# Optimization experiments

Measured on AMD Instinct MI355X. Metric: run time of the kernel, lower is better.

## Reference

```python
import jax, jax.numpy as jnp
import numpy as np

N, B, E = 2048, 2, 1024      # seq_len, batch, embedding_dims
H = 1024                      # hidden_dims
NH, D = 16, 64                # num_heads, head_dim (NH*D == H)
SCALE = 1.0 / float(np.sqrt(H))  # NOTE: module divides by sqrt(hidden_dims), not sqrt(head_dim)


def setup_inputs() -> dict:
    key = jax.random.key(0)
    k0, k1, k2 = jax.random.split(key, 3)
    x = jax.random.normal(k0, (N, B, E), dtype=jnp.float32)
    W_proj = jax.random.normal(k1, (E, 3 * H), dtype=jnp.float32) * 0.02
    b_proj = jnp.zeros((3 * H,), dtype=jnp.float32)
    W_out = jax.random.normal(k2, (H, E), dtype=jnp.float32) * 0.02
    b_out = jnp.zeros((E,), dtype=jnp.float32)
    return {"x": x, "W_proj": W_proj, "b_proj": b_proj, "W_out": W_out, "b_out": b_out}


def reference(x, W_proj, b_proj, W_out, b_out):
    n, b, _ = x.shape
    # QKV projection: [n, b, 3H] -> 'n b (k h d) -> k b h n d'
    proj = x @ W_proj + b_proj
    qkv = proj.reshape(n, b, 3, NH, D).transpose(2, 1, 3, 0, 4)  # [3, b, h, n, d]
    q, k, v = qkv[0], qkv[1], qkv[2]
    # scaled dot-product scores [b, h, n, n]
    scores = jnp.einsum('bhid,bhjd->bhij', q, k) * SCALE
    # causal mask: -inf above the diagonal (generate_square_subsequent_mask)
    i = jnp.arange(n)
    mask = jnp.where(i[None, :] > i[:, None], -jnp.inf, 0.0).astype(scores.dtype)
    att = jax.nn.softmax(scores + mask, axis=-1)  # dropout = identity (eval)
    out = jnp.einsum('bhij,bhjd->bhid', att, v)   # [b, h, n, d]
    out = out.transpose(2, 0, 1, 3).reshape(n, b, H)  # 'b h n d -> n b (h d)'
    return out @ W_out + b_out
```

## Files before the change

### kernel.cpp

```cpp
#include <hip/hip_runtime.h>
#include <cstdint>
#include <cstddef>

typedef __bf16 bf16_t;
typedef __bf16 bf16x8 __attribute__((ext_vector_type(8)));
typedef __bf16 bf16x4 __attribute__((ext_vector_type(4)));
typedef float f32x4 __attribute__((ext_vector_type(4)));

#define N_SEQ 2048
#define BATCH 2
#define EMB   1024
#define HID   1024
#define NHEAD 16
#define HDIM  64
#define NBROW (N_SEQ * BATCH)
#define ATT_SCALE2 (0.03125f * 1.44269504f)

#define EXP2F(x) __builtin_amdgcn_exp2f(x)

static __device__ __forceinline__ void async_copy16(const bf16_t* g, bf16_t* l) {
  __builtin_amdgcn_global_load_lds((const __attribute__((address_space(1))) void*)g,
                                   (__attribute__((address_space(3))) void*)l,
                                   16, 0, 0);
}

__global__ __launch_bounds__(256) void prep_kernel(
    const float* __restrict__ x, const float* __restrict__ Wp,
    const float* __restrict__ Wo, bf16_t* __restrict__ Xb,
    bf16_t* __restrict__ Wpt, bf16_t* __restrict__ Wot) {
  int bid = blockIdx.x;
  if (bid < 4096) {
    int i = (bid * 256 + threadIdx.x) * 4;
    float4 v = *(const float4*)(x + i);
    bf16x4 o;
    o[0] = (bf16_t)v.x; o[1] = (bf16_t)v.y; o[2] = (bf16_t)v.z; o[3] = (bf16_t)v.w;
    *(bf16x4*)(Xb + i) = o;
    return;
  }
  __shared__ float tile[32][33];
  const float* in; bf16_t* out; int R, C, bx;
  if (bid < 4096 + 3072) { bx = bid - 4096; in = Wp; out = Wpt; R = 1024; C = 3072; }
  else                   { bx = bid - 7168; in = Wo; out = Wot; R = 1024; C = 1024; }
  int gx = C / 32;
  int bc = (bx % gx) * 32, br = (bx / gx) * 32;
  int tx = threadIdx.x & 31, ty = threadIdx.x >> 5;
  #pragma unroll
  for (int i = 0; i < 32; i += 8)
    tile[ty + i][tx] = in[(size_t)(br + ty + i) * C + bc + tx];
  __syncthreads();
  #pragma unroll
  for (int i = 0; i < 32; i += 8)
    out[(size_t)(bc + ty + i) * R + br + tx] = (bf16_t)tile[tx][ty + i];
}

__global__ void vt_transpose_kernel(const bf16_t* __restrict__ Pj,
                                    bf16_t* __restrict__ Vt) {
  __shared__ bf16_t tile[32][33];
  int tx = threadIdx.x & 31, ty = threadIdx.x >> 5;
  int n0 = blockIdx.x * 32, d0 = blockIdx.y * 32;
  int bh = blockIdx.z;
  int h = bh & 15, b = bh >> 4;
  const int PJP = 3 * HID;
  #pragma unroll
  for (int i = 0; i < 32; i += 8)
    tile[ty + i][tx] = Pj[(size_t)((n0 + ty + i) * BATCH + b) * PJP + 2 * HID + h * HDIM + d0 + tx];
  __syncthreads();
  #pragma unroll
  for (int i = 0; i < 32; i += 8)
    Vt[(size_t)(bh * HDIM + d0 + ty + i) * N_SEQ + n0 + tx] = tile[tx][ty + i];
}

template <int BM, int BN, int BK, bool OUT_BF16, bool SCALEQ>
__global__ __launch_bounds__(256) void gemm_bt_kernel(
    const bf16_t* __restrict__ A, const bf16_t* __restrict__ Bt,
    const float* __restrict__ bias, void* __restrict__ Cout,
    int M, int Nn, int K) {
  constexpr int MT = BM / 32;
  constexpr int NT = BN / 32;
  constexpr int OCTS = BK / 8;
  constexpr int OM = OCTS - 1;
  __shared__ __align__(16) bf16_t As[BM * BK];
  __shared__ __align__(16) bf16_t Bs[BN * BK];
  int tid = threadIdx.x;
  int wave = tid >> 6, lane = tid & 63;
  int c = lane & 15, quad = lane >> 4;
  int bm = blockIdx.x * BM;
  int bn = blockIdx.y * BN;
  int wm = (wave & 1) * (BM / 2), wn = (wave >> 1) * (BN / 2);
  f32x4 acc[MT][NT] = {};

  for (int kb = 0; kb < K; kb += BK) {
    #pragma unroll
    for (int i = 0; i < BM * OCTS / 256; ++i) {
      int p = i * 256 + tid;
      int row = p >> (OCTS == 8 ? 3 : 4), ko = (p & OM) ^ (row & OM);
      async_copy16(A + (size_t)(bm + row) * K + kb + ko * 8,
                   As + (size_t)(i * 256 + wave * 64) * 8);
    }
    #pragma unroll
    for (int i = 0; i < BN * OCTS / 256; ++i) {
      int p = i * 256 + tid;
      int row = p >> (OCTS == 8 ? 3 : 4), ko = (p & OM) ^ (row & OM);
      async_copy16(Bt + (size_t)(bn + row) * K + kb + ko * 8,
                   Bs + (size_t)(i * 256 + wave * 64) * 8);
    }
    __syncthreads();
    #pragma unroll
    for (int kk = 0; kk < BK / 32; ++kk) {
      bf16x8 af[MT], bf[NT];
      #pragma unroll
      for (int mt = 0; mt < MT; ++mt) {
        int row = wm + mt * 16 + c;
        int slot = (kk * 4 + quad) ^ (row & OM);
        af[mt] = *(const bf16x8*)(As + (size_t)(row * OCTS + slot) * 8);
      }
      #pragma unroll
      for (int nt = 0; nt < NT; ++nt) {
        int row = wn + nt * 16 + c;
        int slot = (kk * 4 + quad) ^ (row & OM);
        bf[nt] = *(const bf16x8*)(Bs + (size_t)(row * OCTS + slot) * 8);
      }
      #pragma unroll
      for (int mt = 0; mt < MT; ++mt)
        #pragma unroll
        for (int nt = 0; nt < NT; ++nt)
          acc[mt][nt] = __builtin_amdgcn_mfma_f32_16x16x32_bf16(
              af[mt], bf[nt], acc[mt][nt], 0, 0, 0);
    }
    __syncthreads();
  }

  #pragma unroll
  for (int nt = 0; nt < NT; ++nt) {
    int col = bn + wn + nt * 16 + c;
    float bv = bias[col];
    float sc = (SCALEQ && col < HID) ? ATT_SCALE2 : 1.0f;
    #pragma unroll
    for (int mt = 0; mt < MT; ++mt) {
      #pragma unroll
      for (int r = 0; r < 4; ++r) {
        int row = bm + wm + mt * 16 + quad * 4 + r;
        float v = (acc[mt][nt][r] + bv) * sc;
        if (OUT_BF16)
          ((bf16_t*)Cout)[(size_t)row * Nn + col] = (bf16_t)v;
        else
          ((float*)Cout)[(size_t)row * Nn + col] = v;
      }
    }
  }
}

__global__ __launch_bounds__(512, 4) void flash_attn_kernel(
    const bf16_t* __restrict__ Pj, const bf16_t* __restrict__ Vt,
    bf16_t* __restrict__ AO) {
  __shared__ __align__(16) bf16_t Ks[2][64 * 64];
  __shared__ __align__(16) bf16_t Vs[2][64 * 64];
  __shared__ __align__(16) bf16_t Ps[8][16 * 64];
  const int PJP = 3 * HID;
  int tid = threadIdx.x, wave = tid >> 6, lane = tid & 63;
  int c = lane & 15, quad = lane >> 4;
  int c7 = c & 7;
  int bid = blockIdx.x;
  int qb = (bid < 256) ? (15 - (bid >> 5)) : ((bid - 256) >> 5);
  int bh = bid & 31;
  int h = bh & 15, b = bh >> 4;
  int i0 = qb * 128;

  int i_row = i0 + wave * 16 + c;
  const bf16_t* qg = Pj + (size_t)(i_row * BATCH + b) * PJP + h * HDIM + quad * 8;
  bf16x8 qf0 = *(const bf16x8*)(qg);
  bf16x8 qf1 = *(const bf16x8*)(qg + 32);

  f32x4 o[4] = {};
  float lrow = 0.f;

  int jr = tid >> 3, oc = tid & 7;
  int lds_off = jr * 64 + (oc ^ (jr & 7)) * 8;
  const bf16_t* kg0 = Pj + (size_t)b * PJP + HID + h * HDIM + oc * 8;
  const bf16_t* vg0 = Vt + (size_t)(bh * HDIM + jr) * N_SEQ + oc * 8;

  int njt = 2 * qb + 2;
  bf16x8 kreg = *(const bf16x8*)(kg0 + (size_t)jr * BATCH * PJP);
  bf16x8 vreg = *(const bf16x8*)(vg0);

  for (int jt = 0; jt < njt; ++jt) {
    bf16_t* ks = Ks[jt & 1];
    bf16_t* vs = Vs[jt & 1];
    *(bf16x8*)(ks + lds_off) = kreg;
    *(bf16x8*)(vs + lds_off) = vreg;
    __syncthreads();
    if (jt + 1 < njt) {
      int j0n = (jt + 1) * 64;
      kreg = *(const bf16x8*)(kg0 + (size_t)(j0n + jr) * BATCH * PJP);
      vreg = *(const bf16x8*)(vg0 + j0n);
    }

    f32x4 st[4];
    #pragma unroll
    for (int mt = 0; mt < 4; ++mt) {
      const bf16_t* kr = ks + (mt * 16 + c) * 64;
      bf16x8 ka0 = *(const bf16x8*)(kr + ((quad) ^ c7) * 8);
      bf16x8 ka1 = *(const bf16x8*)(kr + ((quad + 4) ^ c7) * 8);
      f32x4 s = {};
      s = __builtin_amdgcn_mfma_f32_16x16x32_bf16(ka0, qf0, s, 0, 0, 0);
      st[mt] = __builtin_amdgcn_mfma_f32_16x16x32_bf16(ka1, qf1, s, 0, 0, 0);
    }
    if (jt >= 2 * qb) {
      int j0 = jt * 64;
      int ig = i0 + wave * 16 + c;
      #pragma unroll
      for (int mt = 0; mt < 4; ++mt)
        #pragma unroll
        for (int r = 0; r < 4; ++r)
          if (j0 + mt * 16 + quad * 4 + r > ig) st[mt][r] = -1e30f;
    }

    #pragma unroll
    for (int mt = 0; mt < 4; ++mt)
      #pragma unroll
      for (int r = 0; r < 4; ++r) {
        st[mt][r] = EXP2F(st[mt][r]);
        lrow += st[mt][r];
      }

    bf16_t* pw = Ps[wave];
    #pragma unroll
    for (int mt = 0; mt < 4; ++mt) {
      bf16x4 pv;
      #pragma unroll
      for (int r = 0; r < 4; ++r) pv[r] = (bf16_t)st[mt][r];
      int joct = mt * 2 + (quad >> 1);
      *(bf16x4*)(pw + c * 64 + (joct ^ c7) * 8 + (quad & 1) * 4) = pv;
    }
    const bf16_t* pr = pw + c * 64;
    bf16x8 pa0 = *(const bf16x8*)(pr + ((quad) ^ c7) * 8);
    bf16x8 pa1 = *(const bf16x8*)(pr + ((quad + 4) ^ c7) * 8);

    #pragma unroll
    for (int nt = 0; nt < 4; ++nt) {
      const bf16_t* vr = vs + (nt * 16 + c) * 64;
      bf16x8 vb0 = *(const bf16x8*)(vr + ((quad) ^ c7) * 8);
      bf16x8 vb1 = *(const bf16x8*)(vr + ((quad + 4) ^ c7) * 8);
      o[nt] = __builtin_amdgcn_mfma_f32_16x16x32_bf16(vb0, pa0, o[nt], 0, 0, 0);
      o[nt] = __builtin_amdgcn_mfma_f32_16x16x32_bf16(vb1, pa1, o[nt], 0, 0, 0);
    }
  }

  float lfull = lrow;
  lfull += __shfl_xor(lfull, 16);
  lfull += __shfl_xor(lfull, 32);
  float linv = 1.0f / lfull;
  int orow = (i0 + wave * 16 + c) * BATCH + b;
  #pragma unroll
  for (int nt = 0; nt < 4; ++nt) {
    bf16x4 pv;
    #pragma unroll
    for (int r = 0; r < 4; ++r) pv[r] = (bf16_t)(o[nt][r] * linv);
    *(bf16x4*)(AO + (size_t)orow * HID + h * HDIM + nt * 16 + quad * 4) = pv;
  }
}

extern "C" void kernel_launch(void* const* d_in, const int* in_sizes, int n_in,
                              void* d_out, int out_size, void* d_ws, size_t ws_size,
                              hipStream_t stream) {
  const float* x      = (const float*)d_in[0];
  const float* W_proj = (const float*)d_in[1];
  const float* b_proj = (const float*)d_in[2];
  const float* W_out  = (const float*)d_in[3];
  const float* b_out  = (const float*)d_in[4];

  bf16_t* Xb  = (bf16_t*)d_ws;
  bf16_t* Wpt = Xb  + (size_t)NBROW * EMB;
  bf16_t* Wot = Wpt + (size_t)3 * HID * EMB;
  bf16_t* Pj  = Wot + (size_t)HID * EMB;
  bf16_t* AO  = Pj  + (size_t)NBROW * 3 * HID;
  bf16_t* Vt  = AO  + (size_t)NBROW * HID;

  prep_kernel<<<8192, 256, 0, stream>>>(x, W_proj, W_out, Xb, Wpt, Wot);
  gemm_bt_kernel<128, 64, 64, true, true>
      <<<dim3(NBROW / 128, 3 * HID / 64), 256, 0, stream>>>(
      Xb, Wpt, b_proj, (void*)Pj, NBROW, 3 * HID, EMB);
  vt_transpose_kernel<<<dim3(N_SEQ / 32, HDIM / 32, BATCH * NHEAD), 256, 0, stream>>>(
      Pj, Vt);
  flash_attn_kernel<<<512, 512, 0, stream>>>(Pj, Vt, AO);
  gemm_bt_kernel<64, 64, 128, false, false>
      <<<dim3(NBROW / 64, EMB / 64), 256, 0, stream>>>(
      AO, Wot, b_out, d_out, NBROW, EMB, HID);
}
```

Measured before the change: 169.7 us.

## Double-buffer GEMM shared tiles and prefetch next K-slab during MFMA compute

The bt-GEMM kernel now keeps two LDS buffers for the A and B tiles. It issues the asynchronous global-to-LDS copies for the next K block right after the barrier, so those loads overlap the MFMA work on the current block, and the trailing barrier is dropped. Per-thread global source pointers and LDS offsets are computed once before the loop. BK is fixed at 64, which halves the K tile of the output-projection GEMM (it was 128). The cost is twice the LDS per block, which may reduce occupancy, and the compiler's wait-count placement at the barrier may limit how much the loads actually overlap with compute.

```diff
diff --git a/kernel.cpp b/kernel.cpp
--- a/kernel.cpp
+++ b/kernel.cpp
@@ -70,17 +70,18 @@
     Vt[(size_t)(bh * HDIM + d0 + ty + i) * N_SEQ + n0 + tx] = tile[tx][ty + i];
 }
 
-template <int BM, int BN, int BK, bool OUT_BF16, bool SCALEQ>
+template <int BM, int BN, bool OUT_BF16, bool SCALEQ>
 __global__ __launch_bounds__(256) void gemm_bt_kernel(
     const bf16_t* __restrict__ A, const bf16_t* __restrict__ Bt,
     const float* __restrict__ bias, void* __restrict__ Cout,
     int M, int Nn, int K) {
+  constexpr int BK = 64;
   constexpr int MT = BM / 32;
   constexpr int NT = BN / 32;
-  constexpr int OCTS = BK / 8;
-  constexpr int OM = OCTS - 1;
-  __shared__ __align__(16) bf16_t As[BM * BK];
-  __shared__ __align__(16) bf16_t Bs[BN * BK];
+  constexpr int CA = BM / 32;
+  constexpr int CB = BN / 32;
+  __shared__ __align__(16) bf16_t As[2][BM * BK];
+  __shared__ __align__(16) bf16_t Bs[2][BN * BK];
   int tid = threadIdx.x;
   int wave = tid >> 6, lane = tid & 63;
   int c = lane & 15, quad = lane >> 4;
@@ -89,36 +90,56 @@
   int wm = (wave & 1) * (BM / 2), wn = (wave >> 1) * (BN / 2);
   f32x4 acc[MT][NT] = {};
 
-  for (int kb = 0; kb < K; kb += BK) {
-    #pragma unroll
-    for (int i = 0; i < BM * OCTS / 256; ++i) {
-      int p = i * 256 + tid;
-      int row = p >> (OCTS == 8 ? 3 : 4), ko = (p & OM) ^ (row & OM);
-      async_copy16(A + (size_t)(bm + row) * K + kb + ko * 8,
-                   As + (size_t)(i * 256 + wave * 64) * 8);
-    }
-    #pragma unroll
-    for (int i = 0; i < BN * OCTS / 256; ++i) {
-      int p = i * 256 + tid;
-      int row = p >> (OCTS == 8 ? 3 : 4), ko = (p & OM) ^ (row & OM);
-      async_copy16(Bt + (size_t)(bn + row) * K + kb + ko * 8,
-                   Bs + (size_t)(i * 256 + wave * 64) * 8);
-    }
+  const bf16_t* agp[CA]; int alo[CA];
+  const bf16_t* bgp[CB]; int blo[CB];
+  #pragma unroll
+  for (int i = 0; i < CA; ++i) {
+    int p = i * 256 + tid;
+    int row = p >> 3, ko = (p & 7) ^ (row & 7);
+    agp[i] = A + (size_t)(bm + row) * K + ko * 8;
+    alo[i] = (i * 256 + wave * 64) * 8;
+  }
+  #pragma unroll
+  for (int i = 0; i < CB; ++i) {
+    int p = i * 256 + tid;
+    int row = p >> 3, ko = (p & 7) ^ (row & 7);
+    bgp[i] = Bt + (size_t)(bn + row) * K + ko * 8;
+    blo[i] = (i * 256 + wave * 64) * 8;
+  }
+
+  #pragma unroll
+  for (int i = 0; i < CA; ++i) async_copy16(agp[i], &As[0][alo[i]]);
+  #pragma unroll
+  for (int i = 0; i < CB; ++i) async_copy16(bgp[i], &Bs[0][blo[i]]);
+
+  int nkb = K / BK;
+  for (int ki = 0; ki < nkb; ++ki) {
     __syncthreads();
-    #pragma unroll
-    for (int kk = 0; kk < BK / 32; ++kk) {
+    if (ki + 1 < nkb) {
+      int kb = (ki + 1) * BK;
+      bf16_t* an = As[(ki + 1) & 1];
+      bf16_t* bnx = Bs[(ki + 1) & 1];
+      #pragma unroll
+      for (int i = 0; i < CA; ++i) async_copy16(agp[i] + kb, an + alo[i]);
+      #pragma unroll
+      for (int i = 0; i < CB; ++i) async_copy16(bgp[i] + kb, bnx + blo[i]);
+    }
+    const bf16_t* as = As[ki & 1];
+    const bf16_t* bs = Bs[ki & 1];
+    #pragma unroll
+    for (int kk = 0; kk < 2; ++kk) {
       bf16x8 af[MT], bf[NT];
       #pragma unroll
       for (int mt = 0; mt < MT; ++mt) {
         int row = wm + mt * 16 + c;
-        int slot = (kk * 4 + quad) ^ (row & OM);
-        af[mt] = *(const bf16x8*)(As + (size_t)(row * OCTS + slot) * 8);
+        int slot = (kk * 4 + quad) ^ (row & 7);
+        af[mt] = *(const bf16x8*)(as + (size_t)(row * 8 + slot) * 8);
       }
       #pragma unroll
       for (int nt = 0; nt < NT; ++nt) {
         int row = wn + nt * 16 + c;
-        int slot = (kk * 4 + quad) ^ (row & OM);
-        bf[nt] = *(const bf16x8*)(Bs + (size_t)(row * OCTS + slot) * 8);
+        int slot = (kk * 4 + quad) ^ (row & 7);
+        bf[nt] = *(const bf16x8*)(bs + (size_t)(row * 8 + slot) * 8);
       }
       #pragma unroll
       for (int mt = 0; mt < MT; ++mt)
@@ -127,7 +148,6 @@
           acc[mt][nt] = __builtin_amdgcn_mfma_f32_16x16x32_bf16(
               af[mt], bf[nt], acc[mt][nt], 0, 0, 0);
     }
-    __syncthreads();
   }
 
   #pragma unroll
@@ -277,13 +297,13 @@
   bf16_t* Vt  = AO  + (size_t)NBROW * HID;
 
   prep_kernel<<<8192, 256, 0, stream>>>(x, W_proj, W_out, Xb, Wpt, Wot);
-  gemm_bt_kernel<128, 64, 64, true, true>
+  gemm_bt_kernel<128, 64, true, true>
       <<<dim3(NBROW / 128, 3 * HID / 64), 256, 0, stream>>>(
       Xb, Wpt, b_proj, (void*)Pj, NBROW, 3 * HID, EMB);
   vt_transpose_kernel<<<dim3(N_SEQ / 32, HDIM / 32, BATCH * NHEAD), 256, 0, stream>>>(
       Pj, Vt);
   flash_attn_kernel<<<512, 512, 0, stream>>>(Pj, Vt, AO);
-  gemm_bt_kernel<64, 64, 128, false, false>
+  gemm_bt_kernel<64, 64, false, false>
       <<<dim3(NBROW / 64, EMB / 64), 256, 0, stream>>>(
       AO, Wot, b_out, d_out, NBROW, EMB, HID);
 }
```

Measured after the change: 168.0 us. Within noise of the previous version (-1.0%).
